# Kernel tuning notes

Measured on AMD Instinct MI355X. Metric: run time of the kernel, lower is better.

## Reference

```python
import jax, jax.numpy as jnp
import numpy as np

# --- static hash-grid config (matches tcnn HashGrid in the torch module) ---
DIM = 3
N_LEVELS = 16
F = 2                      # n_features_per_level
LOG2_T = 19
T = 1 << LOG2_T            # hashmap size per level
BASE_RES = 16
TARGET_RES = 2048
PLS = float(np.exp2(np.log2(TARGET_RES / BASE_RES) / (N_LEVELS - 1)))  # per_level_scale
SCALES = [BASE_RES * PLS ** l for l in range(N_LEVELS)]
PRIMES = np.array([1, 2654435761, 805459861], dtype=np.uint32)
# 8 corner offsets of the unit cube, shape [8, 3]
OFFS = np.stack(np.meshgrid(*([np.arange(2)] * DIM), indexing='ij'), -1).reshape(-1, DIM).astype(np.float32)


def _hash(idx_u32):
    # idx_u32: [..., 3] uint32 -> [...] uint32 index into table of size T (power of 2)
    h = idx_u32[..., 0] * jnp.uint32(PRIMES[0])
    h = h ^ (idx_u32[..., 1] * jnp.uint32(PRIMES[1]))
    h = h ^ (idx_u32[..., 2] * jnp.uint32(PRIMES[2]))
    return h & jnp.uint32(T - 1)


def hashgrid_encode(x, table):
    # x: [N, 3] in [0,1); table: [L, T, F] fp32
    outs = []
    offs = jnp.asarray(OFFS)                      # [8, 3]
    for l in range(N_LEVELS):
        pos = x * jnp.float32(SCALES[l])          # [N, 3]
        base = jnp.floor(pos)
        frac = pos - base                         # [N, 3]
        corner = base[:, None, :] + offs[None]    # [N, 8, 3]
        idx = corner.astype(jnp.uint32)
        h = _hash(idx)                            # [N, 8]
        feat = table[l][h]                        # [N, 8, F] (gather)
        # trilinear weights: prod over dims of frac or (1-frac)
        w = jnp.prod(jnp.where(offs[None] > 0.5, frac[:, None, :], 1.0 - frac[:, None, :]), axis=-1)  # [N, 8]
        outs.append(jnp.sum(w[..., None] * feat, axis=1))  # [N, F]
    return jnp.concatenate(outs, axis=-1)         # [N, L*F] = [N, 32]


def setup_inputs() -> dict:
    key = jax.random.key(0)
    ks = jax.random.split(key, 8)
    N = 1048576
    dim_in = N_LEVELS * F          # 32
    hid = 16                       # (16+15)//16*16
    dout = 16                      # grid_output_dim
    x = jax.random.uniform(ks[0], (N, DIM), dtype=jnp.float32)
    table = jax.random.uniform(ks[1], (N_LEVELS, T, F), dtype=jnp.float32, minval=-1e-4, maxval=1e-4)
    def lin(k, fi, fo):
        b = 1.0 / np.sqrt(fi)
        return jax.random.uniform(k, (fo, fi), dtype=jnp.float32, minval=-b, maxval=b)
    W0 = lin(ks[2], dim_in, hid); b0 = jnp.zeros((hid,), jnp.float32)
    W1 = lin(ks[3], hid, hid);    b1 = jnp.zeros((hid,), jnp.float32)
    W2 = lin(ks[4], hid, dout);   b2 = jnp.zeros((dout,), jnp.float32)
    return {"x": x, "table": table, "W0": W0, "b0": b0, "W1": W1, "b1": b1, "W2": W2, "b2": b2}


def reference(x, table, W0, b0, W1, b1, W2, b2):
    h = hashgrid_encode(x, table)                 # [N, 32]
    h = jax.nn.relu(h @ W0.T + b0)
    h = jax.nn.relu(h @ W1.T + b1)
    return h @ W2.T + b2                          # [N, 16]
```

## Files before the change

kernel.cpp:

```cpp
#include <hip/hip_runtime.h>
#include <math.h>

#define NLV 16
#define LOG2_T 19
#define T_SIZE (1u << LOG2_T)
#define T_MASK (T_SIZE - 1u)
#define P2 2654435761u
#define P3 805459861u

typedef float vf2 __attribute__((ext_vector_type(2)));
typedef float vf4 __attribute__((ext_vector_type(4)));

struct Scales { float s[NLV]; };

__device__ __forceinline__ void enc_level(
    float px, float py, float pz, float s, const float* __restrict__ tl,
    float& f0, float& f1)
{
    const float fx = px * s, fy = py * s, fz = pz * s;
    const float bx = floorf(fx), by = floorf(fy), bz = floorf(fz);
    const float rx = fx - bx, ry = fy - by, rz = fz - bz;
    const unsigned ix0 = (unsigned)bx, iy0 = (unsigned)by, iz0 = (unsigned)bz;
    const unsigned hx0 = ix0,      hx1 = ix0 + 1u;
    const unsigned hy0 = iy0 * P2, hy1 = (iy0 + 1u) * P2;
    const unsigned hz0 = iz0 * P3, hz1 = (iz0 + 1u) * P3;
    const float wx0 = 1.f - rx, wy0 = 1.f - ry, wz0 = 1.f - rz;
    f0 = 0.f; f1 = 0.f;
    #pragma unroll
    for (int c = 0; c < 8; ++c) {
        unsigned h = ((c & 4) ? hx1 : hx0) ^ ((c & 2) ? hy1 : hy0) ^ ((c & 1) ? hz1 : hz0);
        h &= T_MASK;
        const vf2 f = *(const vf2*)(tl + 2u * (size_t)h);
        const float w = ((c & 4) ? rx : wx0) * ((c & 2) ? ry : wy0) * ((c & 1) ? rz : wz0);
        f0 += w * f[0];
        f1 += w * f[1];
    }
}

__global__ __launch_bounds__(256) void encode_coarse_kernel(
    const float* __restrict__ x, const float* __restrict__ table,
    float* __restrict__ enc, int N, Scales sc)
{
    int i = blockIdx.x * 256 + threadIdx.x;
    if (i >= N) return;
    const float px = x[3 * (size_t)i + 0];
    const float py = x[3 * (size_t)i + 1];
    const float pz = x[3 * (size_t)i + 2];
    #pragma unroll
    for (int l = 0; l < 5; ++l) {
        float f0, f1;
        enc_level(px, py, pz, sc.s[l], table + (size_t)l * T_SIZE * 2u, f0, f1);
        vf2 v; v[0] = f0; v[1] = f1;
        __builtin_nontemporal_store(v, (vf2*)(enc + ((size_t)l * N + i) * 2u));
    }
}

__global__ __launch_bounds__(256) void encode_one_kernel(
    const float* __restrict__ x, const float* __restrict__ tl, float s,
    float* __restrict__ encl, int N)
{
    int i = blockIdx.x * 256 + threadIdx.x;
    if (i >= N) return;
    const float px = __builtin_nontemporal_load(x + 3 * (size_t)i + 0);
    const float py = __builtin_nontemporal_load(x + 3 * (size_t)i + 1);
    const float pz = __builtin_nontemporal_load(x + 3 * (size_t)i + 2);
    float f0, f1;
    enc_level(px, py, pz, s, tl, f0, f1);
    vf2 v; v[0] = f0; v[1] = f1;
    __builtin_nontemporal_store(v, (vf2*)(encl + (size_t)i * 2u));
}

__global__ __launch_bounds__(256) void mlp_kernel(
    const float* __restrict__ enc,
    const float* __restrict__ W0, const float* __restrict__ b0,
    const float* __restrict__ W1, const float* __restrict__ b1,
    const float* __restrict__ W2, const float* __restrict__ b2,
    float* __restrict__ out, int N)
{
    int i = blockIdx.x * 256 + threadIdx.x;
    if (i >= N) return;

    float e[32];
    #pragma unroll
    for (int l = 0; l < NLV; ++l) {
        vf2 v = __builtin_nontemporal_load((const vf2*)(enc + ((size_t)l * N + i) * 2u));
        e[2 * l + 0] = v[0];
        e[2 * l + 1] = v[1];
    }

    float a0[16];
    #pragma unroll
    for (int j = 0; j < 16; ++j) {
        float s = b0[j];
        #pragma unroll
        for (int k = 0; k < 32; ++k) s += e[k] * W0[j * 32 + k];
        a0[j] = fmaxf(s, 0.f);
    }
    float a1[16];
    #pragma unroll
    for (int j = 0; j < 16; ++j) {
        float s = b1[j];
        #pragma unroll
        for (int k = 0; k < 16; ++k) s += a0[k] * W1[j * 16 + k];
        a1[j] = fmaxf(s, 0.f);
    }
    float o[16];
    #pragma unroll
    for (int j = 0; j < 16; ++j) {
        float s = b2[j];
        #pragma unroll
        for (int k = 0; k < 16; ++k) s += a1[k] * W2[j * 16 + k];
        o[j] = s;
    }

    #pragma unroll
    for (int q = 0; q < 4; ++q) {
        vf4 v; v[0] = o[4*q]; v[1] = o[4*q+1]; v[2] = o[4*q+2]; v[3] = o[4*q+3];
        __builtin_nontemporal_store(v, (vf4*)(out + 16 * (size_t)i + 4 * q));
    }
}

__global__ __launch_bounds__(256) void tcnn_fused_kernel(
    const float* __restrict__ x,
    const float* __restrict__ table,
    const float* __restrict__ W0, const float* __restrict__ b0,
    const float* __restrict__ W1, const float* __restrict__ b1,
    const float* __restrict__ W2, const float* __restrict__ b2,
    float* __restrict__ out, int N, Scales sc)
{
    int i = blockIdx.x * blockDim.x + threadIdx.x;
    if (i >= N) return;
    const float px = x[3 * (size_t)i + 0];
    const float py = x[3 * (size_t)i + 1];
    const float pz = x[3 * (size_t)i + 2];
    float e[32];
    #pragma unroll
    for (int l = 0; l < NLV; ++l) {
        float f0, f1;
        enc_level(px, py, pz, sc.s[l], table + (size_t)l * T_SIZE * 2u, f0, f1);
        e[2 * l] = f0; e[2 * l + 1] = f1;
    }
    float a0[16];
    #pragma unroll
    for (int j = 0; j < 16; ++j) {
        float s = b0[j];
        #pragma unroll
        for (int k = 0; k < 32; ++k) s += e[k] * W0[j * 32 + k];
        a0[j] = fmaxf(s, 0.f);
    }
    float a1[16];
    #pragma unroll
    for (int j = 0; j < 16; ++j) {
        float s = b1[j];
        #pragma unroll
        for (int k = 0; k < 16; ++k) s += a0[k] * W1[j * 16 + k];
        a1[j] = fmaxf(s, 0.f);
    }
    #pragma unroll
    for (int j = 0; j < 16; ++j) {
        float s = b2[j];
        #pragma unroll
        for (int k = 0; k < 16; ++k) s += a1[k] * W2[j * 16 + k];
        out[16 * (size_t)i + j] = s;
    }
}

extern "C" void kernel_launch(void* const* d_in, const int* in_sizes, int n_in,
                              void* d_out, int out_size, void* d_ws, size_t ws_size,
                              hipStream_t stream) {
    const float* x     = (const float*)d_in[0];
    const float* table = (const float*)d_in[1];
    const float* W0    = (const float*)d_in[2];
    const float* b0    = (const float*)d_in[3];
    const float* W1    = (const float*)d_in[4];
    const float* b1    = (const float*)d_in[5];
    const float* W2    = (const float*)d_in[6];
    const float* b2    = (const float*)d_in[7];
    float* out = (float*)d_out;

    const int N = in_sizes[0] / 3;

    Scales sc;
    const double pls = exp2(log2(2048.0 / 16.0) / 15.0);
    for (int l = 0; l < NLV; ++l) sc.s[l] = (float)(16.0 * pow(pls, (double)l));

    const int block = 256;
    const int grid = (N + block - 1) / block;

    const size_t need = (size_t)N * 2u * NLV * sizeof(float);
    if (ws_size >= need) {
        float* enc = (float*)d_ws;
        encode_coarse_kernel<<<grid, block, 0, stream>>>(x, table, enc, N, sc);
        for (int l = 5; l < NLV; ++l) {
            encode_one_kernel<<<grid, block, 0, stream>>>(
                x, table + (size_t)l * T_SIZE * 2u, sc.s[l],
                enc + (size_t)l * (size_t)N * 2u, N);
        }
        mlp_kernel<<<grid, block, 0, stream>>>(enc, W0, b0, W1, b1, W2, b2, out, N);
    } else {
        tcnn_fused_kernel<<<grid, block, 0, stream>>>(x, table, W0, b0, W1, b1, W2, b2,
                                                      out, N, sc);
    }
}
```

Before: 612.0 us.

## Sort points by Morton cell before hash-grid encoding for gather locality

Adds a counting sort of input points into 32^3 Morton-ordered buckets (histogram, single-block scan, atomic scatter) so the encode kernels process spatially nearby points together. This aims to improve cache locality of the hash-table gathers, at least on the coarse levels where neighbouring points share corners. The MLP kernel writes results back through the permutation. Costs are extra passes over x, atomics, a serial single-block scan, and a scattered output store; fine levels with a large hash table may see little reuse.

```diff
diff --git a/kernel.cpp b/kernel.cpp
--- a/kernel.cpp
+++ b/kernel.cpp
@@ -7,11 +7,78 @@
 #define T_MASK (T_SIZE - 1u)
 #define P2 2654435761u
 #define P3 805459861u
+#define NBUCK 32768
 
 typedef float vf2 __attribute__((ext_vector_type(2)));
 typedef float vf4 __attribute__((ext_vector_type(4)));
 
 struct Scales { float s[NLV]; };
+
+__device__ __forceinline__ unsigned mpart(unsigned v) {
+    v = (v | (v << 8)) & 0x100Fu;
+    v = (v | (v << 4)) & 0x10C3u;
+    v = (v | (v << 2)) & 0x1249u;
+    return v;
+}
+__device__ __forceinline__ unsigned mkey(float px, float py, float pz) {
+    unsigned cx = (unsigned)(px * 32.f); cx = cx > 31u ? 31u : cx;
+    unsigned cy = (unsigned)(py * 32.f); cy = cy > 31u ? 31u : cy;
+    unsigned cz = (unsigned)(pz * 32.f); cz = cz > 31u ? 31u : cz;
+    return mpart(cx) | (mpart(cy) << 1) | (mpart(cz) << 2);
+}
+
+__global__ __launch_bounds__(256) void zero_hist_kernel(unsigned* hist) {
+    int i = blockIdx.x * 256 + threadIdx.x;
+    if (i < NBUCK) hist[i] = 0u;
+}
+
+__global__ __launch_bounds__(256) void hist_kernel(
+    const float* __restrict__ x, unsigned* __restrict__ hist, int N)
+{
+    int i = blockIdx.x * 256 + threadIdx.x;
+    if (i >= N) return;
+    const float px = x[3 * (size_t)i + 0];
+    const float py = x[3 * (size_t)i + 1];
+    const float pz = x[3 * (size_t)i + 2];
+    atomicAdd(&hist[mkey(px, py, pz)], 1u);
+}
+
+__global__ __launch_bounds__(1024) void scan_kernel(unsigned* hist) {
+    __shared__ unsigned tot[1024];
+    const int t = threadIdx.x;
+    const unsigned base = (unsigned)t * 32u;
+    unsigned loc[32];
+    unsigned s = 0;
+    #pragma unroll
+    for (int k = 0; k < 32; ++k) { loc[k] = s; s += hist[base + k]; }
+    tot[t] = s;
+    __syncthreads();
+    for (int off = 1; off < 1024; off <<= 1) {
+        unsigned u = (t >= off) ? tot[t - off] : 0u;
+        __syncthreads();
+        tot[t] += u;
+        __syncthreads();
+    }
+    const unsigned excl = tot[t] - s;
+    #pragma unroll
+    for (int k = 0; k < 32; ++k) hist[base + k] = excl + loc[k];
+}
+
+__global__ __launch_bounds__(256) void scatter_kernel(
+    const float* __restrict__ x, unsigned* __restrict__ cursor,
+    vf4* __restrict__ xs, int* __restrict__ perm, int N)
+{
+    int i = blockIdx.x * 256 + threadIdx.x;
+    if (i >= N) return;
+    const float px = x[3 * (size_t)i + 0];
+    const float py = x[3 * (size_t)i + 1];
+    const float pz = x[3 * (size_t)i + 2];
+    const unsigned key = mkey(px, py, pz);
+    const unsigned pos = atomicAdd(&cursor[key], 1u);
+    vf4 v; v[0] = px; v[1] = py; v[2] = pz; v[3] = 0.f;
+    xs[pos] = v;
+    perm[pos] = i;
+}
 
 __device__ __forceinline__ void enc_level(
     float px, float py, float pz, float s, const float* __restrict__ tl,
@@ -38,6 +105,86 @@
 }
 
 __global__ __launch_bounds__(256) void encode_coarse_kernel(
+    const vf4* __restrict__ xs, const float* __restrict__ table,
+    float* __restrict__ enc, int N, Scales sc)
+{
+    int i = blockIdx.x * 256 + threadIdx.x;
+    if (i >= N) return;
+    const vf4 p = xs[i];
+    #pragma unroll
+    for (int l = 0; l < 5; ++l) {
+        float f0, f1;
+        enc_level(p[0], p[1], p[2], sc.s[l], table + (size_t)l * T_SIZE * 2u, f0, f1);
+        vf2 v; v[0] = f0; v[1] = f1;
+        __builtin_nontemporal_store(v, (vf2*)(enc + ((size_t)l * N + i) * 2u));
+    }
+}
+
+__global__ __launch_bounds__(256) void encode_one_kernel(
+    const vf4* __restrict__ xs, const float* __restrict__ tl, float s,
+    float* __restrict__ encl, int N)
+{
+    int i = blockIdx.x * 256 + threadIdx.x;
+    if (i >= N) return;
+    const vf4 p = xs[i];
+    float f0, f1;
+    enc_level(p[0], p[1], p[2], s, tl, f0, f1);
+    vf2 v; v[0] = f0; v[1] = f1;
+    __builtin_nontemporal_store(v, (vf2*)(encl + (size_t)i * 2u));
+}
+
+__global__ __launch_bounds__(256) void mlp_kernel(
+    const float* __restrict__ enc, const int* __restrict__ perm,
+    const float* __restrict__ W0, const float* __restrict__ b0,
+    const float* __restrict__ W1, const float* __restrict__ b1,
+    const float* __restrict__ W2, const float* __restrict__ b2,
+    float* __restrict__ out, int N)
+{
+    int i = blockIdx.x * 256 + threadIdx.x;
+    if (i >= N) return;
+
+    float e[32];
+    #pragma unroll
+    for (int l = 0; l < NLV; ++l) {
+        vf2 v = __builtin_nontemporal_load((const vf2*)(enc + ((size_t)l * N + i) * 2u));
+        e[2 * l + 0] = v[0];
+        e[2 * l + 1] = v[1];
+    }
+
+    float a0[16];
+    #pragma unroll
+    for (int j = 0; j < 16; ++j) {
+        float s = b0[j];
+        #pragma unroll
+        for (int k = 0; k < 32; ++k) s += e[k] * W0[j * 32 + k];
+        a0[j] = fmaxf(s, 0.f);
+    }
+    float a1[16];
+    #pragma unroll
+    for (int j = 0; j < 16; ++j) {
+        float s = b1[j];
+        #pragma unroll
+        for (int k = 0; k < 16; ++k) s += a0[k] * W1[j * 16 + k];
+        a1[j] = fmaxf(s, 0.f);
+    }
+    float o[16];
+    #pragma unroll
+    for (int j = 0; j < 16; ++j) {
+        float s = b2[j];
+        #pragma unroll
+        for (int k = 0; k < 16; ++k) s += a1[k] * W2[j * 16 + k];
+        o[j] = s;
+    }
+
+    float* op = out + 16 * (size_t)perm[i];
+    #pragma unroll
+    for (int q = 0; q < 4; ++q) {
+        vf4 v; v[0] = o[4*q]; v[1] = o[4*q+1]; v[2] = o[4*q+2]; v[3] = o[4*q+3];
+        __builtin_nontemporal_store(v, (vf4*)(op + 4 * q));
+    }
+}
+
+__global__ __launch_bounds__(256) void encode_coarse_unsorted_kernel(
     const float* __restrict__ x, const float* __restrict__ table,
     float* __restrict__ enc, int N, Scales sc)
 {
@@ -54,23 +201,21 @@
         __builtin_nontemporal_store(v, (vf2*)(enc + ((size_t)l * N + i) * 2u));
     }
 }
-
-__global__ __launch_bounds__(256) void encode_one_kernel(
+__global__ __launch_bounds__(256) void encode_one_unsorted_kernel(
     const float* __restrict__ x, const float* __restrict__ tl, float s,
     float* __restrict__ encl, int N)
 {
     int i = blockIdx.x * 256 + threadIdx.x;
     if (i >= N) return;
-    const float px = __builtin_nontemporal_load(x + 3 * (size_t)i + 0);
-    const float py = __builtin_nontemporal_load(x + 3 * (size_t)i + 1);
-    const float pz = __builtin_nontemporal_load(x + 3 * (size_t)i + 2);
+    const float px = x[3 * (size_t)i + 0];
+    const float py = x[3 * (size_t)i + 1];
+    const float pz = x[3 * (size_t)i + 2];
     float f0, f1;
     enc_level(px, py, pz, s, tl, f0, f1);
     vf2 v; v[0] = f0; v[1] = f1;
     __builtin_nontemporal_store(v, (vf2*)(encl + (size_t)i * 2u));
 }
-
-__global__ __launch_bounds__(256) void mlp_kernel(
+__global__ __launch_bounds__(256) void mlp_noperm_kernel(
     const float* __restrict__ enc,
     const float* __restrict__ W0, const float* __restrict__ b0,
     const float* __restrict__ W1, const float* __restrict__ b1,
@@ -79,7 +224,6 @@
 {
     int i = blockIdx.x * 256 + threadIdx.x;
     if (i >= N) return;
-
     float e[32];
     #pragma unroll
     for (int l = 0; l < NLV; ++l) {
@@ -87,7 +231,6 @@
         e[2 * l + 0] = v[0];
         e[2 * l + 1] = v[1];
     }
-
     float a0[16];
     #pragma unroll
     for (int j = 0; j < 16; ++j) {
@@ -104,25 +247,16 @@
         for (int k = 0; k < 16; ++k) s += a0[k] * W1[j * 16 + k];
         a1[j] = fmaxf(s, 0.f);
     }
-    float o[16];
     #pragma unroll
     for (int j = 0; j < 16; ++j) {
         float s = b2[j];
         #pragma unroll
         for (int k = 0; k < 16; ++k) s += a1[k] * W2[j * 16 + k];
-        o[j] = s;
-    }
-
-    #pragma unroll
-    for (int q = 0; q < 4; ++q) {
-        vf4 v; v[0] = o[4*q]; v[1] = o[4*q+1]; v[2] = o[4*q+2]; v[3] = o[4*q+3];
-        __builtin_nontemporal_store(v, (vf4*)(out + 16 * (size_t)i + 4 * q));
-    }
-}
-
+        out[16 * (size_t)i + j] = s;
+    }
+}
 __global__ __launch_bounds__(256) void tcnn_fused_kernel(
-    const float* __restrict__ x,
-    const float* __restrict__ table,
+    const float* __restrict__ x, const float* __restrict__ table,
     const float* __restrict__ W0, const float* __restrict__ b0,
     const float* __restrict__ W1, const float* __restrict__ b1,
     const float* __restrict__ W2, const float* __restrict__ b2,
@@ -187,16 +321,38 @@
     const int block = 256;
     const int grid = (N + block - 1) / block;
 
-    const size_t need = (size_t)N * 2u * NLV * sizeof(float);
-    if (ws_size >= need) {
-        float* enc = (float*)d_ws;
-        encode_coarse_kernel<<<grid, block, 0, stream>>>(x, table, enc, N, sc);
+    const size_t encB  = (size_t)N * 2u * NLV * sizeof(float);
+    const size_t xsB   = (size_t)N * sizeof(float) * 4u;
+    const size_t permB = (size_t)N * sizeof(int);
+    const size_t histB = (size_t)NBUCK * sizeof(unsigned);
+
+    if (ws_size >= encB + xsB + permB + histB) {
+        float*    enc  = (float*)d_ws;
+        vf4*      xs   = (vf4*)((char*)d_ws + encB);
+        int*      perm = (int*)((char*)d_ws + encB + xsB);
+        unsigned* hist = (unsigned*)((char*)d_ws + encB + xsB + permB);
+
+        zero_hist_kernel<<<(NBUCK + 255) / 256, block, 0, stream>>>(hist);
+        hist_kernel<<<grid, block, 0, stream>>>(x, hist, N);
+        scan_kernel<<<1, 1024, 0, stream>>>(hist);
+        scatter_kernel<<<grid, block, 0, stream>>>(x, hist, xs, perm, N);
+
+        encode_coarse_kernel<<<grid, block, 0, stream>>>(xs, table, enc, N, sc);
         for (int l = 5; l < NLV; ++l) {
             encode_one_kernel<<<grid, block, 0, stream>>>(
+                xs, table + (size_t)l * T_SIZE * 2u, sc.s[l],
+                enc + (size_t)l * (size_t)N * 2u, N);
+        }
+        mlp_kernel<<<grid, block, 0, stream>>>(enc, perm, W0, b0, W1, b1, W2, b2, out, N);
+    } else if (ws_size >= encB) {
+        float* enc = (float*)d_ws;
+        encode_coarse_unsorted_kernel<<<grid, block, 0, stream>>>(x, table, enc, N, sc);
+        for (int l = 5; l < NLV; ++l) {
+            encode_one_unsorted_kernel<<<grid, block, 0, stream>>>(
                 x, table + (size_t)l * T_SIZE * 2u, sc.s[l],
                 enc + (size_t)l * (size_t)N * 2u, N);
         }
-        mlp_kernel<<<grid, block, 0, stream>>>(enc, W0, b0, W1, b1, W2, b2, out, N);
+        mlp_noperm_kernel<<<grid, block, 0, stream>>>(enc, W0, b0, W1, b1, W2, b2, out, N);
     } else {
         tcnn_fused_kernel<<<grid, block, 0, stream>>>(x, table, W0, b0, W1, b1, W2, b2,
                                                       out, N, sc);
```

Result: no change. 623.4 us (+1.9%).
